# Performance work log

Measured on AMD Instinct MI355X. Metric: run time of the kernel, lower is better.

The kernel has to match this reference:

```python
import jax, jax.numpy as jnp
import numpy as np

B, S, D_MODEL, D_K, D_V = 8, 2048, 1024, 1024, 1024


def setup_inputs() -> dict:
    key = jax.random.key(0)
    k1, k2, k3, k4 = jax.random.split(key, 4)
    x = jax.random.normal(k1, (B, S, D_MODEL), dtype=jnp.float32)
    # Store projection weights as [d_model, d_out] so projection is x @ W
    # (equivalent to torch Linear(d_model, d_out, bias=False) with W^T).
    scale = 1.0 / np.sqrt(D_MODEL)
    Wq = jax.random.normal(k2, (D_MODEL, D_K), dtype=jnp.float32) * scale
    Wk = jax.random.normal(k3, (D_MODEL, D_K), dtype=jnp.float32) * scale
    Wv = jax.random.normal(k4, (D_MODEL, D_V), dtype=jnp.float32) * scale
    return {"x": x, "Wq": Wq, "Wk": Wk, "Wv": Wv}


def reference(x, Wq, Wk, Wv):
    # Single-head causal self-attention, faithful to the original:
    # NOTE: the original scales by sqrt(x.shape[-1]) == sqrt(d_model),
    # not sqrt(d_k of the projection).
    Q = jnp.einsum('bsd,dk->bsk', x, Wq)
    K = jnp.einsum('bsd,dk->bsk', x, Wk)
    V = jnp.einsum('bsd,dv->bsv', x, Wv)
    inv_scale = 1.0 / jnp.sqrt(jnp.asarray(x.shape[-1], x.dtype))
    A = jnp.einsum('bqk,bsk->bqs', Q, K) * inv_scale  # [B, S, S]
    S_len = A.shape[-1]
    causal = jnp.tril(jnp.ones((S_len, S_len), dtype=bool))  # [S, S]
    A = jnp.where(causal, A, -jnp.inf)
    P = jax.nn.softmax(A, axis=-1)
    return jnp.einsum('bqs,bsv->bqv', P, V)
```

## Files before the change

kernel.cpp:

```cpp
#include <hip/hip_runtime.h>
#include <hip/hip_bf16.h>
#include <stdint.h>


typedef __bf16 bf16_t;
typedef __bf16 bf16x4 __attribute__((ext_vector_type(4)));
typedef __bf16 bf16x8 __attribute__((ext_vector_type(8)));
typedef float  floatx4 __attribute__((ext_vector_type(4)));

#define NB 8
#define SS 2048
#define DD 1024
#define INV_SCALE 0.03125f

__device__ __forceinline__ void async_ld16(const void* g, void* l) {
  __builtin_amdgcn_global_load_lds(
      (const __attribute__((address_space(1))) void*)g,
      (__attribute__((address_space(3))) void*)l, 16, 0, 0);
}

__device__ __forceinline__ void mm256_core(const bf16_t* __restrict__ Ab,
                                           const bf16_t* __restrict__ Bb,
                                           int lda, int ldb, int nt,
                                           bf16_t* sA, bf16_t* sB,
                                           floatx4 acc[8][4]) {
  const int t    = threadIdx.x;
  const int lane = t & 63;
  const int wid  = t >> 6;
  const int wm   = wid >> 2;
  const int wn   = wid & 3;
  const int fm   = lane & 15;
  const int q    = lane >> 4;
  const int co   = (q ^ ((fm >> 1) & 3)) * 8;

  size_t goA[2], goB[2]; int lo[2];
#pragma unroll
  for (int k = 0; k < 2; ++k) {
    const int u   = k * 512 + t;
    const int row = u >> 2;
    const int cg  = (u & 3) ^ ((row >> 1) & 3);
    goA[k] = (size_t)row * lda + cg * 8;
    goB[k] = (size_t)row * ldb + cg * 8;
    lo[k]  = u * 8;
  }

  auto stage = [&](int tile) {
    bf16_t* la = sA + (tile & 3) * 8192;
    bf16_t* lb = sB + (tile & 3) * 8192;
    const size_t ko = (size_t)tile * 32;
    async_ld16(Ab + ko + goA[0], la + lo[0]);
    async_ld16(Ab + ko + goA[1], la + lo[1]);
    async_ld16(Bb + ko + goB[0], lb + lo[0]);
    async_ld16(Bb + ko + goB[1], lb + lo[1]);
  };

  stage(0);
  if (nt > 1) stage(1);
  if (nt > 2) stage(2);

  const int paOff = (wm * 128 + fm) * 32;
  const int pbOff = (wn * 64 + fm) * 32;

  for (int kt = 0; kt < nt; ++kt) {
    if (kt + 3 < nt) {
      stage(kt + 3);
      asm volatile("s_waitcnt vmcnt(12)" ::: "memory");
    } else if (kt + 2 < nt) {
      asm volatile("s_waitcnt vmcnt(8)" ::: "memory");
    } else if (kt + 1 < nt) {
      asm volatile("s_waitcnt vmcnt(4)" ::: "memory");
    } else {
      asm volatile("s_waitcnt vmcnt(0)" ::: "memory");
    }
    __builtin_amdgcn_s_barrier();
    asm volatile("" ::: "memory");

    const bf16_t* pa = sA + (kt & 3) * 8192 + paOff;
    const bf16_t* pb = sB + (kt & 3) * 8192 + pbOff;
    bf16x8 af[8], bv[4];
#pragma unroll
    for (int j = 0; j < 4; ++j) bv[j] = *(const bf16x8*)(pb + j * 512 + co);
#pragma unroll
    for (int i = 0; i < 8; ++i) af[i] = *(const bf16x8*)(pa + i * 512 + co);

    __builtin_amdgcn_s_setprio(1);
#pragma unroll
    for (int i = 0; i < 8; ++i)
#pragma unroll
      for (int j = 0; j < 4; ++j)
        acc[i][j] = __builtin_amdgcn_mfma_f32_16x16x32_bf16(bv[j], af[i], acc[i][j], 0, 0, 0);
    __builtin_amdgcn_s_setprio(0);

    asm volatile("" ::: "memory");
    __builtin_amdgcn_s_barrier();
  }
}

__device__ __forceinline__ void zero_acc8(floatx4 acc[8][4]) {
#pragma unroll
  for (int i = 0; i < 8; ++i)
#pragma unroll
    for (int j = 0; j < 4; ++j)
      acc[i][j] = floatx4{0.f, 0.f, 0.f, 0.f};
}

__device__ __forceinline__ void store_c256_bf16(bf16_t* __restrict__ Cb, int ldc,
                                                floatx4 acc[8][4]) {
  const int lane = threadIdx.x & 63;
  const int wid  = threadIdx.x >> 6;
  const int wm = wid >> 2, wn = wid & 3;
  const int m0 = wm * 128 + (lane & 15);
  const int n0 = wn * 64 + (lane >> 4) * 4;
#pragma unroll
  for (int i = 0; i < 8; ++i)
#pragma unroll
    for (int j = 0; j < 4; ++j) {
      floatx4 a = acc[i][j];
      bf16x4 o = {(bf16_t)a[0], (bf16_t)a[1], (bf16_t)a[2], (bf16_t)a[3]};
      *(bf16x4*)(Cb + (size_t)(m0 + i * 16) * ldc + n0 + j * 16) = o;
    }
}

__device__ __forceinline__ void mm_core(const bf16_t* __restrict__ Ab,
                                        const bf16_t* __restrict__ Bb,
                                        int lda, int ldb, int kTiles,
                                        bf16_t* sA, bf16_t* sB,
                                        floatx4 acc[4][4]) {
  const int t    = threadIdx.x;
  const int lane = t & 63;
  const int wm   = (t >> 6) >> 1;
  const int wn   = (t >> 6) & 1;
  const int fm   = lane & 15;
  const int q    = lane >> 4;
  const int xo   = fm & 7;

  const bf16_t* ga[4]; const bf16_t* gb[4];
  bf16_t* la[4]; bf16_t* lb[4];
#pragma unroll
  for (int k = 0; k < 4; ++k) {
    const int u   = k * 256 + t;
    const int row = u >> 3;
    const int cc  = (u & 7) ^ (row & 7);
    ga[k] = Ab + (size_t)row * lda + cc * 8;
    gb[k] = Bb + (size_t)row * ldb + cc * 8;
    la[k] = sA + u * 8;
    lb[k] = sB + u * 8;
  }

  const bf16_t* pa = sA + (wm * 64 + fm) * 64;
  const bf16_t* pb = sB + (wn * 64 + fm) * 64;

  for (int kt = 0; kt < kTiles; ++kt) {
    const int ko = kt * 64;
#pragma unroll
    for (int k = 0; k < 4; ++k) async_ld16(ga[k] + ko, la[k]);
#pragma unroll
    for (int k = 0; k < 4; ++k) async_ld16(gb[k] + ko, lb[k]);
    __syncthreads();
#pragma unroll
    for (int h = 0; h < 2; ++h) {
      const int co = ((h * 4 + q) ^ xo) * 8;
      bf16x8 af[4], bfr[4];
#pragma unroll
      for (int i = 0; i < 4; ++i) af[i]  = *(const bf16x8*)(pa + i * 1024 + co);
#pragma unroll
      for (int j = 0; j < 4; ++j) bfr[j] = *(const bf16x8*)(pb + j * 1024 + co);
#pragma unroll
      for (int i = 0; i < 4; ++i)
#pragma unroll
        for (int j = 0; j < 4; ++j)
          acc[i][j] = __builtin_amdgcn_mfma_f32_16x16x32_bf16(bfr[j], af[i], acc[i][j], 0, 0, 0);
    }
    __syncthreads();
  }
}

__device__ __forceinline__ void zero_acc(floatx4 acc[4][4]) {
#pragma unroll
  for (int i = 0; i < 4; ++i)
#pragma unroll
    for (int j = 0; j < 4; ++j)
      acc[i][j] = floatx4{0.f, 0.f, 0.f, 0.f};
}


__global__ __launch_bounds__(256) void prep(const float* __restrict__ x,
                                            const float* __restrict__ Wq,
                                            const float* __restrict__ Wk,
                                            const float* __restrict__ Wv,
                                            bf16_t* __restrict__ xb,
                                            bf16_t* __restrict__ Wt) {
  __shared__ float tile[32][33];
  const int bid = blockIdx.x;
  const int t = threadIdx.x;
  if (bid < 16384) {
    size_t i = (size_t)bid * 256 + t;
    float4 v = ((const float4*)x)[i];
    bf16x4 o = {(bf16_t)v.x, (bf16_t)v.y, (bf16_t)v.z, (bf16_t)v.w};
    ((bf16x4*)xb)[i] = o;
  } else {
    const int wb = bid - 16384;
    const int z = wb >> 10;
    const int rem = wb & 1023;
    const float* W = (z == 0) ? Wq : (z == 1 ? Wk : Wv);
    bf16_t* O = Wt + (size_t)z * DD * DD;
    const int ty = t >> 3;
    const int tx = t & 7;
    const int k0 = (rem >> 5) * 32, n0 = (rem & 31) * 32;
    float4 v = *(const float4*)(W + (size_t)(k0 + ty) * DD + n0 + tx * 4);
    tile[ty][tx * 4 + 0] = v.x;
    tile[ty][tx * 4 + 1] = v.y;
    tile[ty][tx * 4 + 2] = v.z;
    tile[ty][tx * 4 + 3] = v.w;
    __syncthreads();
    bf16x4 o = {(bf16_t)tile[tx * 4 + 0][ty], (bf16_t)tile[tx * 4 + 1][ty],
                (bf16_t)tile[tx * 4 + 2][ty], (bf16_t)tile[tx * 4 + 3][ty]};
    *(bf16x4*)(O + (size_t)(n0 + ty) * DD + k0 + tx * 4) = o;
  }
}


__global__ __launch_bounds__(512, 2) void qkproj_gemm(
    const bf16_t* __restrict__ xb, const bf16_t* __restrict__ Wt,
    bf16_t* __restrict__ QKb) {
  __shared__ __attribute__((aligned(16))) bf16_t sA[4 * 8192];
  __shared__ __attribute__((aligned(16))) bf16_t sB[4 * 8192];
  const int mt = blockIdx.x, nt = blockIdx.y;
  const bf16_t* Ab = xb + (size_t)mt * 256 * DD;
  const bf16_t* Bb = Wt + (size_t)nt * 256 * DD;
  bf16_t* Cb = QKb + (size_t)mt * 256 * (2 * DD) + nt * 256;
  floatx4 acc[8][4];
  zero_acc8(acc);
  mm256_core(Ab, Bb, DD, DD, DD / 32, sA, sB, acc);
  store_c256_bf16(Cb, 2 * DD, acc);
}


__global__ __launch_bounds__(512, 2) void vproj_gemm(
    const bf16_t* __restrict__ xb, const bf16_t* __restrict__ Wt,
    bf16_t* __restrict__ VtB) {
  __shared__ __attribute__((aligned(16))) bf16_t sA[4 * 8192];
  __shared__ __attribute__((aligned(16))) bf16_t sB[4 * 8192];
  const int bid = blockIdx.x;
  const int n = bid & 7;
  const int m = (bid >> 3) & 3;
  const int b = bid >> 5;
  const bf16_t* Ab = Wt + (size_t)2 * DD * DD + (size_t)m * 256 * DD;
  const bf16_t* Bb = xb + (size_t)b * SS * DD + (size_t)n * 256 * DD;
  bf16_t* Cb = VtB + (size_t)b * DD * SS + (size_t)m * 256 * SS + n * 256;
  floatx4 acc[8][4];
  zero_acc8(acc);
  mm256_core(Ab, Bb, DD, DD, DD / 32, sA, sB, acc);
  store_c256_bf16(Cb, SS, acc);
}


__global__ __launch_bounds__(256) void qk_p(
    const bf16_t* __restrict__ Q, const bf16_t* __restrict__ K,
    bf16_t* __restrict__ P, float* __restrict__ lpart) {
  const int b  = blockIdx.x & 7;
  const int tt = 135 - (blockIdx.x >> 3);
  int qi = (int)((sqrtf(8.0f * tt + 1.0f) - 1.0f) * 0.5f);
  while ((qi + 1) * (qi + 2) / 2 <= tt) ++qi;
  while (qi * (qi + 1) / 2 > tt) --qi;
  const int ki = tt - qi * (qi + 1) / 2;

  __shared__ __attribute__((aligned(16))) bf16_t sA[128 * 64];
  __shared__ __attribute__((aligned(16))) bf16_t sB[128 * 64];
  __shared__ float reds[2][128];
  const bf16_t* Ab = Q + ((size_t)b * SS + qi * 128) * (size_t)(2 * DD);
  const bf16_t* Bb = K + ((size_t)b * SS + ki * 128) * (size_t)(2 * DD);
  floatx4 acc[4][4];
  zero_acc(acc);
  mm_core(Ab, Bb, 2 * DD, 2 * DD, DD / 64, sA, sB, acc);

  const int lane = threadIdx.x & 63;
  const int wm = (threadIdx.x >> 6) >> 1, wn = (threadIdx.x >> 6) & 1;
  const bool diag = (ki == qi);
  bf16_t* Pb = P + (size_t)b * SS * SS;
  const int qloc0 = wm * 64 + (lane & 15);
  const int kvb0  = wn * 64 + (lane >> 4) * 4;

#pragma unroll
  for (int i = 0; i < 4; ++i) {
    const int qrow = qloc0 + i * 16;
    float partial = 0.f;
#pragma unroll
    for (int j = 0; j < 4; ++j) {
      const int kvb = kvb0 + j * 16;
      floatx4 p;
#pragma unroll
      for (int r = 0; r < 4; ++r) {
        const float s = acc[i][j][r] * INV_SCALE;
        p[r] = (diag && (kvb + r) > qrow) ? 0.f : __expf(s);
        partial += p[r];
      }
      bf16x4 o = {(bf16_t)p[0], (bf16_t)p[1], (bf16_t)p[2], (bf16_t)p[3]};
      *(bf16x4*)(Pb + (size_t)(qi * 128 + qrow) * SS + ki * 128 + kvb) = o;
    }
    partial += __shfl_xor(partial, 16);
    partial += __shfl_xor(partial, 32);
    if ((lane >> 4) == 0) reds[wn][qrow] = partial;
  }
  __syncthreads();
  const int t = threadIdx.x;
  if (t < 128) {
    size_t row = (size_t)b * SS + qi * 128 + t;
    lpart[row * 16 + ki] = reds[0][t] + reds[1][t];
  }
}


__global__ __launch_bounds__(256) void pv_gemm(
    const bf16_t* __restrict__ P, const bf16_t* __restrict__ Vt,
    const float* __restrict__ lpart, float* __restrict__ Out) {
  const int bid = blockIdx.x;
  const int b  = bid & 7;
  const int nj = (bid >> 3) & 7;
  const int qi = 15 - (bid >> 6);

  __shared__ __attribute__((aligned(16))) bf16_t sA[128 * 64];
  __shared__ __attribute__((aligned(16))) bf16_t sB[128 * 64];
  __shared__ float sRl[128];
  const int t = threadIdx.x;
  if (t < 128) {
    const float* lp = lpart + ((size_t)b * SS + qi * 128 + t) * 16;
    float L = 0.f;
    for (int ci = 0; ci <= qi; ++ci) L += lp[ci];
    sRl[t] = 1.0f / L;
  }
  const bf16_t* Ab = P + (size_t)b * SS * SS + (size_t)qi * 128 * SS;
  const bf16_t* Bb = Vt + (size_t)b * DD * SS + (size_t)nj * 128 * SS;
  float* Cb = Out + (size_t)b * SS * DD + (size_t)qi * 128 * DD + nj * 128;
  floatx4 acc[4][4];
  zero_acc(acc);
  mm_core(Ab, Bb, SS, SS, (qi + 1) * 2, sA, sB, acc);
  const int lane = threadIdx.x & 63;
  const int wm = (threadIdx.x >> 6) >> 1, wn = (threadIdx.x >> 6) & 1;
  const int m0 = wm * 64 + (lane & 15);
  const int n0 = wn * 64 + (lane >> 4) * 4;
#pragma unroll
  for (int i2 = 0; i2 < 4; ++i2) {
    const float scale = sRl[m0 + i2 * 16];
    float* crow = Cb + (size_t)(m0 + i2 * 16) * DD + n0;
#pragma unroll
    for (int j = 0; j < 4; ++j) {
      floatx4 o = acc[i2][j];
      o[0] *= scale; o[1] *= scale; o[2] *= scale; o[3] *= scale;
      *(floatx4*)(crow + j * 16) = o;
    }
  }
}


extern "C" void kernel_launch(void* const* d_in, const int* in_sizes, int n_in,
                              void* d_out, int out_size, void* d_ws, size_t ws_size,
                              hipStream_t stream) {
  const float* x  = (const float*)d_in[0];
  const float* Wq = (const float*)d_in[1];
  const float* Wk = (const float*)d_in[2];
  const float* Wv = (const float*)d_in[3];
  float* out = (float*)d_out;

  char* ws = (char*)d_ws;
  bf16_t* xb   = (bf16_t*)(ws);
  bf16_t* Wt   = (bf16_t*)(ws + 33554432ull);
  bf16_t* QKb  = (bf16_t*)(ws + 39845888ull);
  bf16_t* VtB  = (bf16_t*)(ws + 106954752ull);
  bf16_t* Pb   = (bf16_t*)(ws + 140509184ull);
  float*  lpart= (float*)(ws + 207618048ull);
  (void)in_sizes; (void)n_in; (void)out_size; (void)ws_size;

  prep<<<16384 + 3072, 256, 0, stream>>>(x, Wq, Wk, Wv, xb, Wt);
  qkproj_gemm<<<dim3(64, 8), 512, 0, stream>>>(xb, Wt, QKb);
  vproj_gemm<<<256, 512, 0, stream>>>(xb, Wt, VtB);
  qk_p<<<1088, 256, 0, stream>>>(QKb, QKb + DD, Pb, lpart);
  pv_gemm<<<1024, 256, 0, stream>>>(Pb, VtB, lpart, out);
}
```

Measured before the change: 371.7 us.

## Software-pipeline LDS fragment loads across k-tiles in GEMM core loop

```diff
diff --git a/kernel.cpp b/kernel.cpp
--- a/kernel.cpp
+++ b/kernel.cpp
@@ -18,6 +18,9 @@
       (const __attribute__((address_space(1))) void*)g,
       (__attribute__((address_space(3))) void*)l, 16, 0, 0);
 }
+
+#define FULL_BARRIER() do { asm volatile("" ::: "memory"); \
+  __builtin_amdgcn_s_barrier(); asm volatile("" ::: "memory"); } while (0)
 
 __device__ __forceinline__ void mm256_core(const bf16_t* __restrict__ Ab,
                                            const bf16_t* __restrict__ Bb,
@@ -54,45 +57,78 @@
     async_ld16(Bb + ko + goB[1], lb + lo[1]);
   };
 
+  const int paOff = (wm * 128 + fm) * 32;
+  const int pbOff = (wn * 64 + fm) * 32;
+
   stage(0);
   if (nt > 1) stage(1);
-  if (nt > 2) stage(2);
-
-  const int paOff = (wm * 128 + fm) * 32;
-  const int pbOff = (wn * 64 + fm) * 32;
-
-  for (int kt = 0; kt < nt; ++kt) {
-    if (kt + 3 < nt) {
-      stage(kt + 3);
-      asm volatile("s_waitcnt vmcnt(12)" ::: "memory");
-    } else if (kt + 2 < nt) {
+  if (nt > 2) {
+    stage(2);
+    asm volatile("s_waitcnt vmcnt(4)" ::: "memory");
+  } else {
+    asm volatile("s_waitcnt vmcnt(0)" ::: "memory");
+  }
+  FULL_BARRIER();
+
+  bf16x8 afl[4], afh[4], bvA[4], bvB[4];
+  {
+    const bf16_t* pa = sA + paOff;
+    const bf16_t* pb = sB + pbOff;
+#pragma unroll
+    for (int i = 0; i < 4; ++i) afl[i] = *(const bf16x8*)(pa + i * 512 + co);
+#pragma unroll
+    for (int j = 0; j < 4; ++j) bvA[j] = *(const bf16x8*)(pb + j * 512 + co);
+  }
+
+  auto tile_phase = [&](int tt, bf16x8 (&bvU)[4], bf16x8 (&bvL)[4]) {
+    if (tt + 3 < nt) {
+      stage(tt + 3);
       asm volatile("s_waitcnt vmcnt(8)" ::: "memory");
-    } else if (kt + 1 < nt) {
+    } else if (tt + 2 < nt) {
       asm volatile("s_waitcnt vmcnt(4)" ::: "memory");
+    } else if (tt + 1 < nt) {
+      asm volatile("s_waitcnt vmcnt(0)" ::: "memory");
+    }
+    FULL_BARRIER();
+
+    const bf16_t* pa = sA + (tt & 3) * 8192 + paOff;
+#pragma unroll
+    for (int i = 0; i < 4; ++i) afh[i] = *(const bf16x8*)(pa + (4 + i) * 512 + co);
+    asm volatile("s_waitcnt lgkmcnt(4)" ::: "memory");
+    __builtin_amdgcn_sched_barrier(0);
+    __builtin_amdgcn_s_setprio(1);
+#pragma unroll
+    for (int i = 0; i < 4; ++i)
+#pragma unroll
+      for (int j = 0; j < 4; ++j)
+        acc[i][j] = __builtin_amdgcn_mfma_f32_16x16x32_bf16(bvU[j], afl[i], acc[i][j], 0, 0, 0);
+    __builtin_amdgcn_s_setprio(0);
+
+    if (tt + 1 < nt) {
+      const bf16_t* pan = sA + ((tt + 1) & 3) * 8192 + paOff;
+      const bf16_t* pbn = sB + ((tt + 1) & 3) * 8192 + pbOff;
+#pragma unroll
+      for (int i = 0; i < 4; ++i) afl[i] = *(const bf16x8*)(pan + i * 512 + co);
+#pragma unroll
+      for (int j = 0; j < 4; ++j) bvL[j] = *(const bf16x8*)(pbn + j * 512 + co);
+      asm volatile("s_waitcnt lgkmcnt(8)" ::: "memory");
     } else {
-      asm volatile("s_waitcnt vmcnt(0)" ::: "memory");
-    }
-    __builtin_amdgcn_s_barrier();
-    asm volatile("" ::: "memory");
-
-    const bf16_t* pa = sA + (kt & 3) * 8192 + paOff;
-    const bf16_t* pb = sB + (kt & 3) * 8192 + pbOff;
-    bf16x8 af[8], bv[4];
-#pragma unroll
-    for (int j = 0; j < 4; ++j) bv[j] = *(const bf16x8*)(pb + j * 512 + co);
-#pragma unroll
-    for (int i = 0; i < 8; ++i) af[i] = *(const bf16x8*)(pa + i * 512 + co);
-
+      asm volatile("s_waitcnt lgkmcnt(0)" ::: "memory");
+    }
+    __builtin_amdgcn_sched_barrier(0);
     __builtin_amdgcn_s_setprio(1);
 #pragma unroll
-    for (int i = 0; i < 8; ++i)
+    for (int i = 0; i < 4; ++i)
 #pragma unroll
       for (int j = 0; j < 4; ++j)
-        acc[i][j] = __builtin_amdgcn_mfma_f32_16x16x32_bf16(bv[j], af[i], acc[i][j], 0, 0, 0);
+        acc[4 + i][j] = __builtin_amdgcn_mfma_f32_16x16x32_bf16(bvU[j], afh[i], acc[4 + i][j], 0, 0, 0);
     __builtin_amdgcn_s_setprio(0);
-
-    asm volatile("" ::: "memory");
-    __builtin_amdgcn_s_barrier();
+    FULL_BARRIER();
+  };
+
+  for (int tt = 0; tt < nt; tt += 2) {
+    tile_phase(tt,     bvA, bvB);
+    tile_phase(tt + 1, bvB, bvA);
   }
 }
 
```

Result: no change. 373.3 us (+0.4%).
